# Performance work log

Measured on AMD Instinct MI355X. Metric: run time of the kernel, lower is better.

The kernel has to match this reference:

```python
import jax, jax.numpy as jnp
import numpy as np

B, NSM, NLG = 64, 400, 196
SM, LG = 512, 1024
D, H, DH = 4, 16, 64
INNER = H * DH
EPS = 1e-5


def setup_inputs() -> dict:
    key = jax.random.key(0)
    ks = iter(jax.random.split(key, 40))
    def rn(shape, s=0.02):
        return jax.random.normal(next(ks), shape, jnp.float32) * s
    inp = {
        "sm_tokens": rn((B, NSM + 1, SM), 1.0),
        "lg_tokens": rn((B, NLG + 1, LG), 1.0),
    }
    def branch(p, din, dout):
        inp[p + "_pin_w"] = rn((D, din, dout))
        inp[p + "_pin_b"] = jnp.zeros((D, dout), jnp.float32)
        inp[p + "_ng"] = jnp.ones((D, dout), jnp.float32)
        inp[p + "_nb"] = jnp.zeros((D, dout), jnp.float32)
        inp[p + "_wq"] = rn((D, dout, INNER))
        inp[p + "_wkv"] = rn((D, dout, 2 * INNER))
        inp[p + "_wo"] = rn((D, INNER, dout))
        inp[p + "_wob"] = jnp.zeros((D, dout), jnp.float32)
        inp[p + "_pout_w"] = rn((D, dout, din))
        inp[p + "_pout_b"] = jnp.zeros((D, din), jnp.float32)
    branch("a", SM, LG)   # sm_attend_lg: project sm->lg, attention in lg_dim
    branch("b", LG, SM)   # lg_attend_sm: project lg->sm, attention in sm_dim
    return inp


def _attn(cls_tok, ctx, ng, nb, wq, wkv, wo, wob):
    # cls_tok: [B,1,dim]; ctx: [B,S,dim]. Matches lucidrains cross_vit Attention:
    # LayerNorm(x) first; kv context = concat(normed_x, context); context NOT normed.
    scale = DH ** -0.5
    mu = cls_tok.mean(-1, keepdims=True)
    var = ((cls_tok - mu) ** 2).mean(-1, keepdims=True)
    xn = (cls_tok - mu) * jax.lax.rsqrt(var + EPS) * ng + nb
    c = jnp.concatenate([xn, ctx], axis=1)             # kv_include_self=True
    q = (xn @ wq).reshape(B, 1, H, DH)
    k, v = jnp.split(c @ wkv, 2, axis=-1)
    k = k.reshape(B, -1, H, DH)
    v = v.reshape(B, -1, H, DH)
    s = jnp.einsum('bqhd,bkhd->bhqk', q, k) * scale     # [B,H,1,S+1]
    p = jax.nn.softmax(s, axis=-1)
    o = jnp.einsum('bhqk,bkhd->bqhd', p, v).reshape(B, 1, INNER)
    return o @ wo + wob


def _forward(sm_tokens, lg_tokens,
             a_pin_w, a_pin_b, a_ng, a_nb, a_wq, a_wkv, a_wo, a_wob, a_pout_w, a_pout_b,
             b_pin_w, b_pin_b, b_ng, b_nb, b_wq, b_wkv, b_wo, b_wob, b_pout_w, b_pout_b):
    sm_cls, sm_patch = sm_tokens[:, :1], sm_tokens[:, 1:]
    lg_cls, lg_patch = lg_tokens[:, :1], lg_tokens[:, 1:]
    for i in range(D):
        x = sm_cls @ a_pin_w[i] + a_pin_b[i]
        x = _attn(x, lg_patch, a_ng[i], a_nb[i], a_wq[i], a_wkv[i], a_wo[i], a_wob[i])
        sm_cls = x @ a_pout_w[i] + a_pout_b[i] + sm_cls
        y = lg_cls @ b_pin_w[i] + b_pin_b[i]
        y = _attn(y, sm_patch, b_ng[i], b_nb[i], b_wq[i], b_wkv[i], b_wo[i], b_wob[i])
        lg_cls = y @ b_pout_w[i] + b_pout_b[i] + lg_cls
    sm_out = jnp.concatenate([sm_cls, sm_patch], axis=1)
    lg_out = jnp.concatenate([lg_cls, lg_patch], axis=1)
    return sm_out, lg_out


def reference(sm_tokens, lg_tokens,
              a_pin_w, a_pin_b, a_ng, a_nb, a_wq, a_wkv, a_wo, a_wob, a_pout_w, a_pout_b,
              b_pin_w, b_pin_b, b_ng, b_nb, b_wq, b_wkv, b_wo, b_wob, b_pout_w, b_pout_b):
    return _forward(sm_tokens, lg_tokens,
                    a_pin_w, a_pin_b, a_ng, a_nb, a_wq, a_wkv, a_wo, a_wob, a_pout_w, a_pout_b,
                    b_pin_w, b_pin_b, b_ng, b_nb, b_wq, b_wkv, b_wo, b_wob, b_pout_w, b_pout_b)
```

## Files before the change

### kernel.cpp

```cpp
#include <hip/hip_runtime.h>
#include <hip/hip_bf16.h>
#include <math.h>

#define B_     64
#define NSM_   400
#define NLG_   196
#define SM_    512
#define LG_    1024
#define H_     16
#define DH_    64
#define INNER_ 1024
#define SSTR   424
#define PSTR   424

typedef __attribute__((ext_vector_type(8))) short bf16x8;
typedef __attribute__((ext_vector_type(8))) unsigned short u16x8;
typedef __attribute__((ext_vector_type(4))) float f32x4;

__device__ __forceinline__ unsigned short f2b(float f) {
  unsigned u = __float_as_uint(f);
  u = u + 0x7FFFu + ((u >> 16) & 1u);
  return (unsigned short)(u >> 16);
}
__device__ __forceinline__ f32x4 zero4() {
  f32x4 a; a[0] = 0.f; a[1] = 0.f; a[2] = 0.f; a[3] = 0.f; return a;
}


struct CC2 { const float* tok; float* out; unsigned short* abf; float* cls;
             unsigned short* clsb; int Np1, nf4, shift, tot4; };
struct WTDesc { const float* src; unsigned short* dstT; unsigned short* dstS;
                int K, Ntiles, srcStride, colOff; };
struct WTArgs { WTDesc d[12]; int cum[13]; };
__global__ __launch_bounds__(256) void setup1(CC2 ca, CC2 cb, WTArgs W, int nw,
                                              unsigned short* zb) {
  __shared__ unsigned short tile[64][68];
  const int tid = threadIdx.x;
  if (blockIdx.x == 0) {
    ushort4 z; z.x = 0; z.y = 0; z.z = 0; z.w = 0;
    ((ushort4*)zb)[tid] = z;
  }
  if ((int)blockIdx.x < nw) {
    int bx = blockIdx.x, di = 0;
    while (bx >= W.cum[di + 1]) di++;
    int local = bx - W.cum[di];
    WTDesc g = W.d[di];
    int tn = g.Ntiles;
    int tpl = tn * (g.K >> 6);
    int layer = local / tpl, rem = local % tpl;
    int kt = (rem / tn) * 64, nt = (rem % tn) * 64;
    const float* wp = g.src + (size_t)layer * g.K * g.srcStride;
    unsigned short* dS = g.dstS ? g.dstS + (size_t)layer * g.K * 1024 : nullptr;
    if (!g.dstT) {
#pragma unroll
      for (int p = 0; p < 4; p++) {
        int r = (tid >> 4) + p * 16;
        int c = (tid & 15) * 4;
        const f32x4 v = __builtin_nontemporal_load(
            (const f32x4*)&wp[(size_t)(kt + r) * g.srcStride + g.colOff + nt + c]);
        ushort4 w4;
        w4.x = f2b(v.x); w4.y = f2b(v.y); w4.z = f2b(v.z); w4.w = f2b(v.w);
        *(ushort4*)&dS[(size_t)(kt + r) * 1024 + nt + c] = w4;
      }
    } else {
      unsigned short* op = g.dstT + (size_t)layer * (g.Ntiles * 64) * g.K;
#pragma unroll
      for (int p = 0; p < 4; p++) {
        int r = (tid >> 4) + p * 16;
        int c = (tid & 15) * 4;
        const f32x4 v = __builtin_nontemporal_load(
            (const f32x4*)&wp[(size_t)(kt + r) * g.srcStride + g.colOff + nt + c]);
        ushort4 w4;
        w4.x = f2b(v.x); w4.y = f2b(v.y); w4.z = f2b(v.z); w4.w = f2b(v.w);
        *(ushort4*)&tile[r][c] = w4;
        if (dS) *(ushort4*)&dS[(size_t)(kt + r) * 1024 + nt + c] = w4;
      }
      __syncthreads();
      const int r2 = tid >> 2, cseg = tid & 3;
      u16x8 v0, v1;
#pragma unroll
      for (int i = 0; i < 8; i++) v0[i] = tile[cseg * 16 + i][r2];
#pragma unroll
      for (int i = 0; i < 8; i++) v1[i] = tile[cseg * 16 + 8 + i][r2];
      unsigned short* orow = &op[(size_t)(nt + r2) * g.K + kt + cseg * 16];
      *(u16x8*)&orow[0] = v0;
      *(u16x8*)&orow[8] = v1;
    }
  } else {
    const int nblk = gridDim.x - nw;
    const int total = ca.tot4 + cb.tot4;
    for (int i = ((int)blockIdx.x - nw) * 256 + tid; i < total; i += nblk * 256) {
      CC2 g; int idx;
      if (i < ca.tot4) { g = ca; idx = i; } else { g = cb; idx = i - ca.tot4; }
      int rowg = idx >> g.shift, t = idx & ((1 << g.shift) - 1);
      int bb = rowg / g.Np1, row = rowg - bb * g.Np1;
      const f32x4 v = __builtin_nontemporal_load(&((const f32x4*)g.tok)[idx]);
      __builtin_nontemporal_store(v, &((f32x4*)g.out)[idx]);
      ushort4 w2; w2.x = f2b(v.x); w2.y = f2b(v.y); w2.z = f2b(v.z); w2.w = f2b(v.w);
      if (row > 0) {
        ((ushort4*)g.abf)[(size_t)(bb * (g.Np1 - 1) + row - 1) * g.nf4 + t] = w2;
      } else {
        ((f32x4*)g.cls)[(size_t)bb * g.nf4 + t] = v;
        ((ushort4*)g.clsb)[(size_t)bb * g.nf4 + t] = w2;
      }
    }
  }
}

struct TXArgs { const unsigned short* xbf; unsigned short* xT; int Nctx, dout, xstride, nx, ny, nblk; };
__global__ __launch_bounds__(256) void setup2(TXArgs ta, TXArgs tb) {
  __shared__ unsigned short tile[64][68];
  TXArgs g; int bx = blockIdx.x;
  if (bx < ta.nblk) { g = ta; } else { g = tb; bx -= ta.nblk; }
  int cx = bx % g.nx; int rem = bx / g.nx;
  int jy = rem % g.ny; int b = rem / g.ny;
  int jt = jy * 64, ct = cx * 64;
  const int tid = threadIdx.x;
#pragma unroll
  for (int p = 0; p < 4; p++) {
    int row = (tid >> 4) + p * 16;
    int c = (tid & 15) * 4;
    int j = jt + row;
    ushort4 v;
    if (j < g.Nctx) v = *(const ushort4*)&g.xbf[((size_t)b * g.Nctx + j) * g.dout + ct + c];
    else { v.x = 0; v.y = 0; v.z = 0; v.w = 0; }
    *(ushort4*)&tile[row][c] = v;
  }
  __syncthreads();
  const int r2 = tid >> 2, jseg = tid & 3;
  if (jt + jseg * 16 < g.xstride) {
    u16x8 v0, v1;
#pragma unroll
    for (int i = 0; i < 8; i++) v0[i] = tile[jseg * 16 + i][r2];
#pragma unroll
    for (int i = 0; i < 8; i++) v1[i] = tile[jseg * 16 + 8 + i][r2];
    unsigned short* orow = &g.xT[((size_t)b * g.dout + ct + r2) * g.xstride + jt + jseg * 16];
    *(u16x8*)&orow[0] = v0;
    *(u16x8*)&orow[8] = v1;
  }
}

struct SGDesc {
  const unsigned short* A; const unsigned short* WT; const float* bias;
  float* Cf; unsigned short* Cbf; const float* Rf;
  int K, N;
  float* outF; int ostride;
};
struct SGArgs { SGDesc d[4]; int cum[5]; int nd; };
__global__ __launch_bounds__(256) void sg_wide(SGArgs W) {
  int bx = blockIdx.x, di = 0;
  while (di < W.nd - 1 && bx >= W.cum[di + 1]) di++;
  SGDesc g = W.d[di];
  const int n0 = (bx - W.cum[di]) * 16;
  const int tid = threadIdx.x;
  const int lane = tid & 63, mt = tid >> 6;
  const int r16 = lane & 15, kv8 = (lane >> 4) * 8;
  f32x4 acc0 = zero4(), acc1 = zero4();
  const unsigned short* wp = &g.WT[(size_t)(n0 + r16) * g.K + kv8];
  const unsigned short* ap = &g.A[(size_t)(mt * 16 + r16) * g.K + kv8];
  const int K = g.K;
#pragma unroll 2
  for (int k0 = 0; k0 < K; k0 += 64) {
    acc0 = __builtin_amdgcn_mfma_f32_16x16x32_bf16(*(const bf16x8*)&ap[k0],
                                                   *(const bf16x8*)&wp[k0], acc0, 0, 0, 0);
    acc1 = __builtin_amdgcn_mfma_f32_16x16x32_bf16(*(const bf16x8*)&ap[k0 + 32],
                                                   *(const bf16x8*)&wp[k0 + 32], acc1, 0, 0, 0);
  }
  const int rbase = (lane >> 4) * 4;
#pragma unroll
  for (int rr = 0; rr < 4; rr++) {
    int r = mt * 16 + rbase + rr, c = n0 + r16;
    float v = acc0[rr] + acc1[rr];
    if (g.bias) v += g.bias[c];
    if (g.Rf) v += g.Rf[(size_t)r * g.N + c];
    if (g.Cf)  g.Cf[(size_t)r * g.N + c] = v;
    if (g.Cbf) g.Cbf[(size_t)r * g.N + c] = f2b(v);
    if (g.outF) g.outF[(size_t)r * g.ostride + c] = v;
  }
}

struct LNArgs { const float* x; unsigned short* xnb; const float* ng; const float* nb;
                int dim; unsigned short* xT; int xstr, jcls; };
__global__ __launch_bounds__(256) void ln2(LNArgs la, LNArgs lb) {
  LNArgs g = ((int)blockIdx.x < 64) ? la : lb;
  int b = blockIdx.x & 63, t = threadIdx.x;
  __shared__ float rs[4], rq[4], bc[2];
  const float* xp = g.x + (size_t)b * g.dim;
  float s = 0.f, sq = 0.f;
  for (int c = t; c < g.dim; c += 256) {
    float v = xp[c];
    s += v; sq += v * v;
  }
#pragma unroll
  for (int off = 32; off >= 1; off >>= 1) {
    s += __shfl_down(s, off);
    sq += __shfl_down(sq, off);
  }
  int w = t >> 6;
  if ((t & 63) == 0) { rs[w] = s; rq[w] = sq; }
  __syncthreads();
  if (t == 0) {
    float ts = rs[0] + rs[1] + rs[2] + rs[3];
    float tq = rq[0] + rq[1] + rq[2] + rq[3];
    float mu = ts / g.dim;
    float var = tq / g.dim - mu * mu;
    bc[0] = mu; bc[1] = rsqrtf(var + 1e-5f);
  }
  __syncthreads();
  float mu = bc[0], r = bc[1];
  for (int c = t; c < g.dim; c += 256) {
    unsigned short hv = f2b((xp[c] - mu) * r * g.ng[c] + g.nb[c]);
    g.xnb[(size_t)b * g.dim + c] = hv;
    g.xT[((size_t)b * g.dim + c) * g.xstr + g.jcls] = hv;
  }
}

struct QTArgs { const unsigned short* qb16; const unsigned short* wkvnb;
                unsigned short* qt; int dout, ntiles, nblk; };
__global__ __launch_bounds__(256) void qtilde3(QTArgs ga, QTArgs gb) {
  QTArgs g; int bx = blockIdx.x;
  if (bx < ga.nblk) g = ga; else { g = gb; bx -= ga.nblk; }
  const int h = bx / g.ntiles, nt = bx - h * g.ntiles;
  const int n0 = nt * 16;
  const int tid = threadIdx.x, lane = tid & 63, mt = tid >> 6;
  const int r16 = lane & 15, kv8 = (lane >> 4) * 8;
  const unsigned short* ap = g.qb16 + (size_t)(mt * 16 + r16) * INNER_ + h * 64 + kv8;
  const unsigned short* bp = g.wkvnb + (size_t)(n0 + r16) * 1024 + h * 64 + kv8;
  f32x4 acc0 = zero4(), acc1 = zero4();
  acc0 = __builtin_amdgcn_mfma_f32_16x16x32_bf16(*(const bf16x8*)&ap[0],
                                                 *(const bf16x8*)&bp[0], acc0, 0, 0, 0);
  acc1 = __builtin_amdgcn_mfma_f32_16x16x32_bf16(*(const bf16x8*)&ap[32],
                                                 *(const bf16x8*)&bp[32], acc1, 0, 0, 0);
  const int rbase = (lane >> 4) * 4;
#pragma unroll
  for (int rr = 0; rr < 4; rr++) {
    int b = mt * 16 + rbase + rr;
    g.qt[((size_t)b * 16 + h) * g.dout + n0 + r16] = f2b(acc0[rr] + acc1[rr]);
  }
}

struct SArgs { const unsigned short* qt; const unsigned short* xbf;
               const unsigned short* xnb; const unsigned short* zb; float* S;
               int dout, Nctx, ntj, nbj, nblk; };
__global__ __launch_bounds__(256) void s_gemm(SArgs ga, SArgs gb) {
  SArgs g; int bx;
  if ((int)blockIdx.x < ga.nblk) { g = ga; bx = blockIdx.x; }
  else { g = gb; bx = blockIdx.x - ga.nblk; }
  const int per8 = g.nblk >> 3;
  const int logical = (bx & 7) * per8 + (bx >> 3);
  const int b = logical / g.nbj, jq = logical - b * g.nbj;
  const int tid = threadIdx.x, lane = tid & 63, w = tid >> 6;
  const int jt = jq * 4 + w;
  if (jt >= g.ntj) return;
  const int r16 = lane & 15, kv8 = (lane >> 4) * 8;
  const int j = jt * 16 + r16;
  const unsigned short* brow;
  if (j < g.Nctx)       brow = g.xbf + ((size_t)b * g.Nctx + j) * g.dout;
  else if (j == g.Nctx) brow = g.xnb + (size_t)b * g.dout;
  else                  brow = g.zb;
  const unsigned short* ap = g.qt + ((size_t)b * 16 + r16) * g.dout + kv8;
  const unsigned short* bp = brow + kv8;
  f32x4 acc0 = zero4(), acc1 = zero4();
  const int K = g.dout;
#pragma unroll 2
  for (int k0 = 0; k0 < K; k0 += 64) {
    acc0 = __builtin_amdgcn_mfma_f32_16x16x32_bf16(*(const bf16x8*)&ap[k0],
                                                   *(const bf16x8*)&bp[k0], acc0, 0, 0, 0);
    acc1 = __builtin_amdgcn_mfma_f32_16x16x32_bf16(*(const bf16x8*)&ap[k0 + 32],
                                                   *(const bf16x8*)&bp[k0 + 32], acc1, 0, 0, 0);
  }
  const int rbase = (lane >> 4) * 4;
#pragma unroll
  for (int rr = 0; rr < 4; rr++)
    g.S[((size_t)b * 16 + rbase + rr) * SSTR + jt * 16 + r16] = acc0[rr] + acc1[rr];
}

struct SMArgs { const float* S; unsigned short* p; int Nk, Npad; };
__global__ __launch_bounds__(256) void softmax_p2(SMArgs ga, SMArgs gb) {
  SMArgs g = blockIdx.z ? gb : ga;
  const int h = blockIdx.x, b = blockIdx.y;
  const int t = threadIdx.x;
  __shared__ float red[4];
  const float* Sp = g.S + ((size_t)b * 16 + h) * SSTR;

  float sraw[2] = {-1e30f, -1e30f};
#pragma unroll
  for (int u2 = 0; u2 < 2; u2++) {
    int j = t + u2 * 256;
    if (j < g.Nk) sraw[u2] = Sp[j] * 0.125f;
  }
  float mx = fmaxf(sraw[0], sraw[1]);
#pragma unroll
  for (int o = 32; o >= 1; o >>= 1) mx = fmaxf(mx, __shfl_down(mx, o));
  if ((t & 63) == 0) red[t >> 6] = mx;
  __syncthreads();
  mx = fmaxf(fmaxf(red[0], red[1]), fmaxf(red[2], red[3]));
  __syncthreads();

  float e0 = (t < g.Nk) ? expf(sraw[0] - mx) : 0.f;
  float e1 = (t + 256 < g.Nk) ? expf(sraw[1] - mx) : 0.f;
  float ls = e0 + e1;
#pragma unroll
  for (int o = 32; o >= 1; o >>= 1) ls += __shfl_down(ls, o);
  if ((t & 63) == 0) red[t >> 6] = ls;
  __syncthreads();
  const float denom = red[0] + red[1] + red[2] + red[3];
  const float inv = 1.f / denom;

  unsigned short* pp = g.p + ((size_t)b * 16 + h) * PSTR;
  if (t < g.Nk) pp[t] = f2b(e0 * inv);
  if (t + 256 < g.Nk) pp[t + 256] = f2b(e1 * inv);
  for (int j = g.Nk + t; j < g.Npad; j += 256) pp[j] = 0;
}

struct UG { const unsigned short* p; const unsigned short* xT; unsigned short* u;
            int dout, Npad, xstride, ntx; };
__global__ __launch_bounds__(256) void ugemm2(UG ga, UG gb) {
  const int bid = blockIdx.x;
  const int logical = (bid & 7) * 192 + (bid >> 3);
  const int b = logical / 24;
  int x = logical - b * 24;
  UG g;
  if (x < ga.ntx) g = ga; else { g = gb; x -= ga.ntx; }
  const int tid = threadIdx.x, lane = tid & 63, w = tid >> 6;
  const int c0 = x * 64 + w * 16;
  const int r16 = lane & 15, kv8 = (lane >> 4) * 8, rbase = (lane >> 4) * 4;
  const unsigned short* ap = g.p + ((size_t)b * 16 + r16) * PSTR + kv8;
  const unsigned short* bp = g.xT + ((size_t)b * g.dout + c0 + r16) * g.xstride + kv8;
  f32x4 acc0 = zero4(), acc1 = zero4();
  const int Kp = g.Npad;
  int k0 = 0;
  for (; k0 + 64 <= Kp; k0 += 64) {
    acc0 = __builtin_amdgcn_mfma_f32_16x16x32_bf16(*(const bf16x8*)&ap[k0],
                                                   *(const bf16x8*)&bp[k0], acc0, 0, 0, 0);
    acc1 = __builtin_amdgcn_mfma_f32_16x16x32_bf16(*(const bf16x8*)&ap[k0 + 32],
                                                   *(const bf16x8*)&bp[k0 + 32], acc1, 0, 0, 0);
  }
  if (k0 < Kp)
    acc0 = __builtin_amdgcn_mfma_f32_16x16x32_bf16(*(const bf16x8*)&ap[k0],
                                                   *(const bf16x8*)&bp[k0], acc0, 0, 0, 0);
#pragma unroll
  for (int rr = 0; rr < 4; rr++)
    g.u[((size_t)b * 16 + rbase + rr) * g.dout + c0 + r16] = f2b(acc0[rr] + acc1[rr]);
}

struct OArgs {
  const unsigned short* u; const unsigned short* WTv; unsigned short* ob; int dout;
};
__global__ __launch_bounds__(256) void ogemm_w(OArgs ga, OArgs gb) {
  OArgs g; int bx = blockIdx.x;
  if (bx < 64) { g = ga; } else { g = gb; bx -= 64; }
  const int h = bx >> 2, dt = bx & 3;
  const int tid = threadIdx.x, lane = tid & 63, mt = tid >> 6;
  const int r16 = lane & 15, kv8 = (lane >> 4) * 8;
  const int dout = g.dout;
  f32x4 acc0 = zero4(), acc1 = zero4();
  const unsigned short* wp = &g.WTv[(size_t)(h * 64 + dt * 16 + r16) * dout + kv8];
  const unsigned short* up = &g.u[((size_t)(mt * 16 + r16) * 16 + h) * dout + kv8];
#pragma unroll 2
  for (int k0 = 0; k0 < dout; k0 += 64) {
    acc0 = __builtin_amdgcn_mfma_f32_16x16x32_bf16(*(const bf16x8*)&up[k0],
                                                   *(const bf16x8*)&wp[k0], acc0, 0, 0, 0);
    acc1 = __builtin_amdgcn_mfma_f32_16x16x32_bf16(*(const bf16x8*)&up[k0 + 32],
                                                   *(const bf16x8*)&wp[k0 + 32], acc1, 0, 0, 0);
  }
  const int rbase = (lane >> 4) * 4;
#pragma unroll
  for (int rr = 0; rr < 4; rr++) {
    int bi = mt * 16 + rbase + rr;
    int d = h * 64 + dt * 16 + r16;
    g.ob[(size_t)bi * INNER_ + d] = f2b(acc0[rr] + acc1[rr]);
  }
}

extern "C" void kernel_launch(void* const* d_in, const int* in_sizes, int n_in,
                              void* d_out, int out_size, void* d_ws, size_t ws_size,
                              hipStream_t stream) {
  const float* sm_tokens = (const float*)d_in[0];
  const float* lg_tokens = (const float*)d_in[1];
  const float* a_pin_w  = (const float*)d_in[2];  const float* a_pin_b  = (const float*)d_in[3];
  const float* a_ng     = (const float*)d_in[4];  const float* a_nb     = (const float*)d_in[5];
  const float* a_wq     = (const float*)d_in[6];  const float* a_wkv    = (const float*)d_in[7];
  const float* a_wo     = (const float*)d_in[8];  const float* a_wob    = (const float*)d_in[9];
  const float* a_pout_w = (const float*)d_in[10]; const float* a_pout_b = (const float*)d_in[11];
  const float* b_pin_w  = (const float*)d_in[12]; const float* b_pin_b  = (const float*)d_in[13];
  const float* b_ng     = (const float*)d_in[14]; const float* b_nb     = (const float*)d_in[15];
  const float* b_wq     = (const float*)d_in[16]; const float* b_wkv    = (const float*)d_in[17];
  const float* b_wo     = (const float*)d_in[18]; const float* b_wob    = (const float*)d_in[19];
  const float* b_pout_w = (const float*)d_in[20]; const float* b_pout_b = (const float*)d_in[21];

  float* out = (float*)d_out;
  char* ws = (char*)d_ws;
  size_t off = 0;
  auto alloc = [&](size_t bytes) -> void* {
    void* pt = ws + off;
    off += (bytes + 255) & ~(size_t)255;
    return pt;
  };
  unsigned short* Abf_lg = (unsigned short*)alloc(((size_t)B_ * NLG_ + 32) * LG_ * 2);
  unsigned short* Abf_sm = (unsigned short*)alloc(((size_t)B_ * NSM_ + 32) * SM_ * 2);
  unsigned short* xT_lg  = (unsigned short*)alloc((size_t)B_ * LG_ * 224 * 2);
  unsigned short* xT_sm  = (unsigned short*)alloc((size_t)B_ * SM_ * 416 * 2);
  unsigned short* WTv_a  = (unsigned short*)alloc((size_t)4 * 1024 * LG_ * 2);
  unsigned short* WTv_b  = (unsigned short*)alloc((size_t)4 * 1024 * SM_ * 2);
  unsigned short* wkvnb_a = (unsigned short*)alloc((size_t)4 * LG_ * 1024 * 2);
  unsigned short* wkvnb_b = (unsigned short*)alloc((size_t)4 * SM_ * 1024 * 2);
  unsigned short* WTpin_a = (unsigned short*)alloc((size_t)4 * SM_ * LG_ * 2);
  unsigned short* WTpin_b = (unsigned short*)alloc((size_t)4 * LG_ * SM_ * 2);
  unsigned short* WTwq_a  = (unsigned short*)alloc((size_t)4 * LG_ * INNER_ * 2);
  unsigned short* WTwq_b  = (unsigned short*)alloc((size_t)4 * SM_ * INNER_ * 2);
  unsigned short* WTwo_a  = (unsigned short*)alloc((size_t)4 * INNER_ * LG_ * 2);
  unsigned short* WTwo_b  = (unsigned short*)alloc((size_t)4 * INNER_ * SM_ * 2);
  unsigned short* WTpout_a = (unsigned short*)alloc((size_t)4 * LG_ * SM_ * 2);
  unsigned short* WTpout_b = (unsigned short*)alloc((size_t)4 * SM_ * LG_ * 2);
  unsigned short* qt_a = (unsigned short*)alloc((size_t)B_ * 16 * LG_ * 2);
  unsigned short* qt_b = (unsigned short*)alloc((size_t)B_ * 16 * SM_ * 2);
  float* S_a = (float*)alloc((size_t)B_ * 16 * SSTR * 4);
  float* S_b = (float*)alloc((size_t)B_ * 16 * SSTR * 4);
  unsigned short* p_a = (unsigned short*)alloc((size_t)B_ * 16 * PSTR * 2);
  unsigned short* p_b = (unsigned short*)alloc((size_t)B_ * 16 * PSTR * 2);
  unsigned short* u_a  = (unsigned short*)alloc((size_t)B_ * 16 * LG_ * 2);
  unsigned short* u_b  = (unsigned short*)alloc((size_t)B_ * 16 * SM_ * 2);
  float* cls_sm = (float*)alloc((size_t)B_ * SM_ * 4);
  float* cls_lg = (float*)alloc((size_t)B_ * LG_ * 4);
  unsigned short* clsb_sm = (unsigned short*)alloc((size_t)B_ * SM_ * 2);
  unsigned short* clsb_lg = (unsigned short*)alloc((size_t)B_ * LG_ * 2);
  float* xbuf_a = (float*)alloc((size_t)B_ * LG_ * 4);
  float* xbuf_b = (float*)alloc((size_t)B_ * SM_ * 4);
  unsigned short* xnb_a = (unsigned short*)alloc((size_t)B_ * LG_ * 2);
  unsigned short* xnb_b = (unsigned short*)alloc((size_t)B_ * SM_ * 2);
  float* qbuf_a = (float*)alloc((size_t)B_ * INNER_ * 4);
  float* qbuf_b = (float*)alloc((size_t)B_ * INNER_ * 4);
  unsigned short* qb16_a = (unsigned short*)alloc((size_t)B_ * INNER_ * 2);
  unsigned short* qb16_b = (unsigned short*)alloc((size_t)B_ * INNER_ * 2);
  unsigned short* obufb_a = (unsigned short*)alloc((size_t)B_ * INNER_ * 2);
  unsigned short* obufb_b = (unsigned short*)alloc((size_t)B_ * INNER_ * 2);
  unsigned short* t1b_a = (unsigned short*)alloc((size_t)B_ * LG_ * 2);
  unsigned short* t1b_b = (unsigned short*)alloc((size_t)B_ * SM_ * 2);
  unsigned short* zb = (unsigned short*)alloc(1024 * 2);
  (void)ws_size; (void)in_sizes; (void)n_in; (void)out_size;

  const size_t sm_elems = (size_t)B_ * (NSM_ + 1) * SM_;

  CC2 ca{sm_tokens, out, Abf_sm, cls_sm, clsb_sm, NSM_ + 1, SM_ / 4, 7,
         (int)(sm_elems / 4)};
  CC2 cb{lg_tokens, out + sm_elems, Abf_lg, cls_lg, clsb_lg, NLG_ + 1, LG_ / 4, 8,
         (int)((size_t)B_ * (NLG_ + 1) * LG_ / 4)};
  WTArgs W;
  W.d[0]  = {a_wkv,    nullptr,  wkvnb_a, LG_,   16, 2048, 0};
  W.d[1]  = {a_wkv,    WTv_a,    nullptr, LG_,   16, 2048, 1024};
  W.d[2]  = {b_wkv,    nullptr,  wkvnb_b, SM_,   16, 2048, 0};
  W.d[3]  = {b_wkv,    WTv_b,    nullptr, SM_,   16, 2048, 1024};
  W.d[4]  = {a_pin_w,  WTpin_a,  nullptr, SM_,   16, 1024, 0};
  W.d[5]  = {b_pin_w,  WTpin_b,  nullptr, LG_,    8,  512, 0};
  W.d[6]  = {a_wq,     WTwq_a,   nullptr, LG_,   16, 1024, 0};
  W.d[7]  = {b_wq,     WTwq_b,   nullptr, SM_,   16, 1024, 0};
  W.d[8]  = {a_wo,     WTwo_a,   nullptr, INNER_,16, 1024, 0};
  W.d[9]  = {b_wo,     WTwo_b,   nullptr, INNER_, 8,  512, 0};
  W.d[10] = {a_pout_w, WTpout_a, nullptr, LG_,    8,  512, 0};
  W.d[11] = {b_pout_w, WTpout_b, nullptr, SM_,   16, 1024, 0};
  W.cum[0] = 0;
  for (int i = 0; i < 12; i++)
    W.cum[i + 1] = W.cum[i] + (W.d[i].K / 64) * W.d[i].Ntiles * 4;
  setup1<<<W.cum[12] + 2048, 256, 0, stream>>>(ca, cb, W, W.cum[12], zb);
  TXArgs txa{Abf_lg, xT_lg, NLG_, LG_, 224, LG_ / 64, 4, B_ * (LG_ / 64) * 4};
  TXArgs txb{Abf_sm, xT_sm, NSM_, SM_, 416, SM_ / 64, 7, B_ * (SM_ / 64) * 7};
  setup2<<<txa.nblk + txb.nblk, 256, 0, stream>>>(txa, txb);

  for (int l = 0; l < 4; l++) {
    const unsigned short* WTpin_al = WTpin_a + (size_t)l * SM_ * LG_;
    const unsigned short* WTpin_bl = WTpin_b + (size_t)l * LG_ * SM_;
    const unsigned short* WTwq_al  = WTwq_a  + (size_t)l * LG_ * INNER_;
    const unsigned short* WTwq_bl  = WTwq_b  + (size_t)l * SM_ * INNER_;
    const unsigned short* WTv_al   = WTv_a   + (size_t)l * 1024 * LG_;
    const unsigned short* WTv_bl   = WTv_b   + (size_t)l * 1024 * SM_;
    const unsigned short* wkvnb_al = wkvnb_a + (size_t)l * LG_ * 1024;
    const unsigned short* wkvnb_bl = wkvnb_b + (size_t)l * SM_ * 1024;
    const unsigned short* WTwo_al  = WTwo_a  + (size_t)l * INNER_ * LG_;
    const unsigned short* WTwo_bl  = WTwo_b  + (size_t)l * INNER_ * SM_;
    const unsigned short* WTpout_al = WTpout_a + (size_t)l * LG_ * SM_;
    const unsigned short* WTpout_bl = WTpout_b + (size_t)l * SM_ * LG_;

    SGArgs Gp; Gp.nd = 2;
    Gp.d[0] = {clsb_sm, WTpin_al, a_pin_b + (size_t)l * LG_, xbuf_a, nullptr, nullptr, SM_, LG_, nullptr, 0};
    Gp.d[1] = {clsb_lg, WTpin_bl, b_pin_b + (size_t)l * SM_, xbuf_b, nullptr, nullptr, LG_, SM_, nullptr, 0};
    Gp.cum[0] = 0; Gp.cum[1] = LG_ / 16; Gp.cum[2] = LG_ / 16 + SM_ / 16;
    sg_wide<<<Gp.cum[2], 256, 0, stream>>>(Gp);
    LNArgs la{xbuf_a, xnb_a, a_ng + (size_t)l * LG_, a_nb + (size_t)l * LG_, LG_, xT_lg, 224, NLG_};
    LNArgs lb{xbuf_b, xnb_b, b_ng + (size_t)l * SM_, b_nb + (size_t)l * SM_, SM_, xT_sm, 416, NSM_};
    ln2<<<128, 256, 0, stream>>>(la, lb);
    SGArgs Gq; Gq.nd = 2;
    Gq.d[0] = {xnb_a, WTwq_al, nullptr, qbuf_a, qb16_a, nullptr, LG_, INNER_, nullptr, 0};
    Gq.d[1] = {xnb_b, WTwq_bl, nullptr, qbuf_b, qb16_b, nullptr, SM_, INNER_, nullptr, 0};
    Gq.cum[0] = 0; Gq.cum[1] = 64; Gq.cum[2] = 128;
    sg_wide<<<128, 256, 0, stream>>>(Gq);
    QTArgs qa{qb16_a, wkvnb_al, qt_a, LG_, LG_ / 16, 16 * (LG_ / 16)};
    QTArgs qb{qb16_b, wkvnb_bl, qt_b, SM_, SM_ / 16, 16 * (SM_ / 16)};
    qtilde3<<<qa.nblk + qb.nblk, 256, 0, stream>>>(qa, qb);
    SArgs sa{qt_a, Abf_lg, xnb_a, zb, S_a, LG_, NLG_, 14, 4, B_ * 4};
    SArgs sb{qt_b, Abf_sm, xnb_b, zb, S_b, SM_, NSM_, 26, 7, B_ * 7};
    s_gemm<<<sa.nblk + sb.nblk, 256, 0, stream>>>(sa, sb);
    SMArgs ma{S_a, p_a, NLG_ + 1, 224};
    SMArgs mb{S_b, p_b, NSM_ + 1, 416};
    softmax_p2<<<dim3(H_, B_, 2), 256, 0, stream>>>(ma, mb);
    UG ua{p_a, xT_lg, u_a, LG_, 224, 224, LG_ / 64};
    UG ub{p_b, xT_sm, u_b, SM_, 416, 416, SM_ / 64};
    ugemm2<<<1536, 256, 0, stream>>>(ua, ub);
    OArgs oa{u_a, WTv_al, obufb_a, LG_};
    OArgs ob{u_b, WTv_bl, obufb_b, SM_};
    ogemm_w<<<128, 256, 0, stream>>>(oa, ob);
    SGArgs Gw; Gw.nd = 2;
    Gw.d[0] = {obufb_a, WTwo_al, a_wob + (size_t)l * LG_, nullptr, t1b_a, nullptr, INNER_, LG_, nullptr, 0};
    Gw.d[1] = {obufb_b, WTwo_bl, b_wob + (size_t)l * SM_, nullptr, t1b_b, nullptr, INNER_, SM_, nullptr, 0};
    Gw.cum[0] = 0; Gw.cum[1] = LG_ / 16; Gw.cum[2] = LG_ / 16 + SM_ / 16;
    sg_wide<<<Gw.cum[2], 256, 0, stream>>>(Gw);
    float* outF_a = (l == 3) ? out : nullptr;
    float* outF_b = (l == 3) ? out + sm_elems : nullptr;
    SGArgs Gr; Gr.nd = 2;
    Gr.d[0] = {t1b_a, WTpout_al, a_pout_b + (size_t)l * SM_, cls_sm, clsb_sm, cls_sm, LG_, SM_,
               outF_a, (NSM_ + 1) * SM_};
    Gr.d[1] = {t1b_b, WTpout_bl, b_pout_b + (size_t)l * LG_, cls_lg, clsb_lg, cls_lg, SM_, LG_,
               outF_b, (NLG_ + 1) * LG_};
    Gr.cum[0] = 0; Gr.cum[1] = SM_ / 16; Gr.cum[2] = SM_ / 16 + LG_ / 16;
    sg_wide<<<Gr.cum[2], 256, 0, stream>>>(Gr);
  }
}
```

Before: 473.3 us.

## Widen setup transpose tiles, fold softmax scale into q-tilde, drop unused fp32 q

The weight and context transpose kernels now handle 128-row K tiles per block, so each thread writes 64-byte output runs and the grid is roughly halved. Transposed weights no longer also write the straight copy. The attention scale is applied once in qtilde3 instead of per score in softmax, and the unused fp32 q buffer write is removed. This trades more shared memory per block and fewer blocks for wider stores, and applying the scale before the bf16 rounding slightly changes numerics.

```diff
diff --git a/kernel.cpp b/kernel.cpp
--- a/kernel.cpp
+++ b/kernel.cpp
@@ -34,7 +34,7 @@
 struct WTArgs { WTDesc d[12]; int cum[13]; };
 __global__ __launch_bounds__(256) void setup1(CC2 ca, CC2 cb, WTArgs W, int nw,
                                               unsigned short* zb) {
-  __shared__ unsigned short tile[64][68];
+  __shared__ unsigned short tile[128][68];
   const int tid = threadIdx.x;
   if (blockIdx.x == 0) {
     ushort4 z; z.x = 0; z.y = 0; z.z = 0; z.w = 0;
@@ -46,12 +46,12 @@
     int local = bx - W.cum[di];
     WTDesc g = W.d[di];
     int tn = g.Ntiles;
-    int tpl = tn * (g.K >> 6);
-    int layer = local / tpl, rem = local % tpl;
-    int kt = (rem / tn) * 64, nt = (rem % tn) * 64;
-    const float* wp = g.src + (size_t)layer * g.K * g.srcStride;
-    unsigned short* dS = g.dstS ? g.dstS + (size_t)layer * g.K * 1024 : nullptr;
     if (!g.dstT) {
+      int tpl = tn * (g.K >> 6);
+      int layer = local / tpl, rem = local % tpl;
+      int kt = (rem / tn) * 64, nt = (rem % tn) * 64;
+      const float* wp = g.src + (size_t)layer * g.K * g.srcStride;
+      unsigned short* dS = g.dstS + (size_t)layer * g.K * 1024;
 #pragma unroll
       for (int p = 0; p < 4; p++) {
         int r = (tid >> 4) + p * 16;
@@ -63,9 +63,13 @@
         *(ushort4*)&dS[(size_t)(kt + r) * 1024 + nt + c] = w4;
       }
     } else {
+      int tpl = tn * (g.K >> 7);
+      int layer = local / tpl, rem = local % tpl;
+      int kt = (rem / tn) * 128, nt = (rem % tn) * 64;
+      const float* wp = g.src + (size_t)layer * g.K * g.srcStride;
       unsigned short* op = g.dstT + (size_t)layer * (g.Ntiles * 64) * g.K;
 #pragma unroll
-      for (int p = 0; p < 4; p++) {
+      for (int p = 0; p < 8; p++) {
         int r = (tid >> 4) + p * 16;
         int c = (tid & 15) * 4;
         const f32x4 v = __builtin_nontemporal_load(
@@ -73,18 +77,17 @@
         ushort4 w4;
         w4.x = f2b(v.x); w4.y = f2b(v.y); w4.z = f2b(v.z); w4.w = f2b(v.w);
         *(ushort4*)&tile[r][c] = w4;
-        if (dS) *(ushort4*)&dS[(size_t)(kt + r) * 1024 + nt + c] = w4;
       }
       __syncthreads();
-      const int r2 = tid >> 2, cseg = tid & 3;
-      u16x8 v0, v1;
-#pragma unroll
-      for (int i = 0; i < 8; i++) v0[i] = tile[cseg * 16 + i][r2];
-#pragma unroll
-      for (int i = 0; i < 8; i++) v1[i] = tile[cseg * 16 + 8 + i][r2];
-      unsigned short* orow = &op[(size_t)(nt + r2) * g.K + kt + cseg * 16];
-      *(u16x8*)&orow[0] = v0;
-      *(u16x8*)&orow[8] = v1;
+      const int r2 = tid >> 2, kseg = tid & 3;
+      unsigned short* orow = &op[(size_t)(nt + r2) * g.K + kt + kseg * 32];
+#pragma unroll
+      for (int s = 0; s < 4; s++) {
+        u16x8 v;
+#pragma unroll
+        for (int i = 0; i < 8; i++) v[i] = tile[kseg * 32 + s * 8 + i][r2];
+        *(u16x8*)&orow[s * 8] = v;
+      }
     }
   } else {
     const int nblk = gridDim.x - nw;
@@ -109,15 +112,15 @@
 
 struct TXArgs { const unsigned short* xbf; unsigned short* xT; int Nctx, dout, xstride, nx, ny, nblk; };
 __global__ __launch_bounds__(256) void setup2(TXArgs ta, TXArgs tb) {
-  __shared__ unsigned short tile[64][68];
+  __shared__ unsigned short tile[128][68];
   TXArgs g; int bx = blockIdx.x;
   if (bx < ta.nblk) { g = ta; } else { g = tb; bx -= ta.nblk; }
   int cx = bx % g.nx; int rem = bx / g.nx;
   int jy = rem % g.ny; int b = rem / g.ny;
-  int jt = jy * 64, ct = cx * 64;
+  int jt = jy * 128, ct = cx * 64;
   const int tid = threadIdx.x;
 #pragma unroll
-  for (int p = 0; p < 4; p++) {
+  for (int p = 0; p < 8; p++) {
     int row = (tid >> 4) + p * 16;
     int c = (tid & 15) * 4;
     int j = jt + row;
@@ -127,16 +130,16 @@
     *(ushort4*)&tile[row][c] = v;
   }
   __syncthreads();
-  const int r2 = tid >> 2, jseg = tid & 3;
-  if (jt + jseg * 16 < g.xstride) {
-    u16x8 v0, v1;
-#pragma unroll
-    for (int i = 0; i < 8; i++) v0[i] = tile[jseg * 16 + i][r2];
-#pragma unroll
-    for (int i = 0; i < 8; i++) v1[i] = tile[jseg * 16 + 8 + i][r2];
-    unsigned short* orow = &g.xT[((size_t)b * g.dout + ct + r2) * g.xstride + jt + jseg * 16];
-    *(u16x8*)&orow[0] = v0;
-    *(u16x8*)&orow[8] = v1;
+  const int r2 = tid >> 2, kseg = tid & 3;
+  if (jt + kseg * 32 + 32 <= g.xstride) {
+    unsigned short* orow = &g.xT[((size_t)b * g.dout + ct + r2) * g.xstride + jt + kseg * 32];
+#pragma unroll
+    for (int s = 0; s < 4; s++) {
+      u16x8 v;
+#pragma unroll
+      for (int i = 0; i < 8; i++) v[i] = tile[kseg * 32 + s * 8 + i][r2];
+      *(u16x8*)&orow[s * 8] = v;
+    }
   }
 }
 
@@ -235,7 +238,7 @@
 #pragma unroll
   for (int rr = 0; rr < 4; rr++) {
     int b = mt * 16 + rbase + rr;
-    g.qt[((size_t)b * 16 + h) * g.dout + n0 + r16] = f2b(acc0[rr] + acc1[rr]);
+    g.qt[((size_t)b * 16 + h) * g.dout + n0 + r16] = f2b((acc0[rr] + acc1[rr]) * 0.125f);
   }
 }
 
@@ -287,7 +290,7 @@
 #pragma unroll
   for (int u2 = 0; u2 < 2; u2++) {
     int j = t + u2 * 256;
-    if (j < g.Nk) sraw[u2] = Sp[j] * 0.125f;
+    if (j < g.Nk) sraw[u2] = Sp[j];
   }
   float mx = fmaxf(sraw[0], sraw[1]);
 #pragma unroll
@@ -429,8 +432,6 @@
   float* xbuf_b = (float*)alloc((size_t)B_ * SM_ * 4);
   unsigned short* xnb_a = (unsigned short*)alloc((size_t)B_ * LG_ * 2);
   unsigned short* xnb_b = (unsigned short*)alloc((size_t)B_ * SM_ * 2);
-  float* qbuf_a = (float*)alloc((size_t)B_ * INNER_ * 4);
-  float* qbuf_b = (float*)alloc((size_t)B_ * INNER_ * 4);
   unsigned short* qb16_a = (unsigned short*)alloc((size_t)B_ * INNER_ * 2);
   unsigned short* qb16_b = (unsigned short*)alloc((size_t)B_ * INNER_ * 2);
   unsigned short* obufb_a = (unsigned short*)alloc((size_t)B_ * INNER_ * 2);
@@ -460,11 +461,13 @@
   W.d[10] = {a_pout_w, WTpout_a, nullptr, LG_,    8,  512, 0};
   W.d[11] = {b_pout_w, WTpout_b, nullptr, SM_,   16, 1024, 0};
   W.cum[0] = 0;
-  for (int i = 0; i < 12; i++)
-    W.cum[i + 1] = W.cum[i] + (W.d[i].K / 64) * W.d[i].Ntiles * 4;
+  for (int i = 0; i < 12; i++) {
+    int kb = W.d[i].dstT ? (W.d[i].K / 128) : (W.d[i].K / 64);
+    W.cum[i + 1] = W.cum[i] + kb * W.d[i].Ntiles * 4;
+  }
   setup1<<<W.cum[12] + 2048, 256, 0, stream>>>(ca, cb, W, W.cum[12], zb);
-  TXArgs txa{Abf_lg, xT_lg, NLG_, LG_, 224, LG_ / 64, 4, B_ * (LG_ / 64) * 4};
-  TXArgs txb{Abf_sm, xT_sm, NSM_, SM_, 416, SM_ / 64, 7, B_ * (SM_ / 64) * 7};
+  TXArgs txa{Abf_lg, xT_lg, NLG_, LG_, 224, LG_ / 64, 2, B_ * (LG_ / 64) * 2};
+  TXArgs txb{Abf_sm, xT_sm, NSM_, SM_, 416, SM_ / 64, 4, B_ * (SM_ / 64) * 4};
   setup2<<<txa.nblk + txb.nblk, 256, 0, stream>>>(txa, txb);
 
   for (int l = 0; l < 4; l++) {
@@ -490,8 +493,8 @@
     LNArgs lb{xbuf_b, xnb_b, b_ng + (size_t)l * SM_, b_nb + (size_t)l * SM_, SM_, xT_sm, 416, NSM_};
     ln2<<<128, 256, 0, stream>>>(la, lb);
     SGArgs Gq; Gq.nd = 2;
-    Gq.d[0] = {xnb_a, WTwq_al, nullptr, qbuf_a, qb16_a, nullptr, LG_, INNER_, nullptr, 0};
-    Gq.d[1] = {xnb_b, WTwq_bl, nullptr, qbuf_b, qb16_b, nullptr, SM_, INNER_, nullptr, 0};
+    Gq.d[0] = {xnb_a, WTwq_al, nullptr, nullptr, qb16_a, nullptr, LG_, INNER_, nullptr, 0};
+    Gq.d[1] = {xnb_b, WTwq_bl, nullptr, nullptr, qb16_b, nullptr, SM_, INNER_, nullptr, 0};
     Gq.cum[0] = 0; Gq.cum[1] = 64; Gq.cum[2] = 128;
     sg_wide<<<128, 256, 0, stream>>>(Gq);
     QTArgs qa{qb16_a, wkvnb_al, qt_a, LG_, LG_ / 16, 16 * (LG_ / 16)};
```

Measured after the change: 484.5 us. 2.4% more time.
